# Kernel optimization log

Hardware: AMD Instinct MI355X
Metric: run time of the kernel (lower is better)

## Reference

```python
import jax, jax.numpy as jnp
import numpy as np

NEG = -9.0e15
D = 768


def _init_params(key, d):
    ks = jax.random.split(key, 12)
    s = 0.02
    p = {}
    p['Wa'] = jax.random.normal(ks[0], (d, 1), jnp.float32) * s
    p['ba'] = jnp.zeros((1,), jnp.float32)
    for i, name in enumerate(['qs', 'ks', 'qc', 'kc', 'qr', 'kr']):
        p['W' + name] = jax.random.normal(ks[1 + i], (d, d), jnp.float32) * s
        p['b' + name] = jnp.zeros((d,), jnp.float32)
    p['Wf1'] = jax.random.normal(ks[8], (3 * d, d), jnp.float32) * s
    p['bf1'] = jnp.zeros((d,), jnp.float32)
    p['Wf2'] = jax.random.normal(ks[9], (d, d), jnp.float32) * s
    p['bf2'] = jnp.zeros((d,), jnp.float32)
    p['gamma'] = jnp.ones((d,), jnp.float32)
    p['beta'] = jnp.zeros((d,), jnp.float32)
    return p


def setup_inputs() -> dict:
    key = jax.random.key(0)
    k1, k2, k3 = jax.random.split(key, 3)
    B, L = 8, 1024
    inp = {
        'x': jax.random.normal(k1, (B, L, D), jnp.float32),
        'x_ids': jax.random.randint(k2, (B, L), 0, 1000, jnp.int64 if jax.config.read('jax_enable_x64') else jnp.int32).astype(jnp.int32),
        'pad_idx': 0,
    }
    inp.update(_init_params(k3, D))
    return inp


def _forward(x, x_ids, pad_idx, Wa, ba, Wqs, bqs, Wks, bks, Wqc, bqc, Wkc, bkc,
             Wqr, bqr, Wkr, bkr, Wf1, bf1, Wf2, bf2, gamma, beta):
    B, L, d = x.shape
    valid = x_ids != pad_idx                             # [B,L]
    valid_len = valid.sum(axis=1)
    sep_pos = jnp.clip(valid_len // 2, 1, max(1, L - 2))  # [B]
    pos = jnp.arange(L)[None, :]                          # [1,L]
    false_mask = (pos < sep_pos[:, None]) & valid         # [B,L]
    option_mask = (pos > sep_pos[:, None]) & valid        # [B,L]

    # anomaly gate over false segment
    a_logits = (x @ Wa + ba)[..., 0]                      # [B,L]
    a_logits = jnp.where(false_mask, a_logits, NEG)
    gate = jax.nn.softmax(a_logits, axis=1) * false_mask.astype(x.dtype)
    gate = gate / jnp.clip(gate.sum(axis=1, keepdims=True), 1e-8)

    scale = 1.0 / jnp.sqrt(jnp.asarray(d, x.dtype))
    q_sup, k_sup = x @ Wqs + bqs, x @ Wks + bks
    q_con, k_con = x @ Wqc + bqc, x @ Wkc + bkc
    q_rep, k_rep = x @ Wqr + bqr, x @ Wkr + bkr

    sup_s = jnp.einsum('bld,bmd->blm', q_sup, k_sup) * scale
    con_s = jnp.einsum('bld,bmd->blm', q_con, k_con) * scale
    rep_s = jnp.einsum('bld,bmd->blm', q_rep, k_rep) * scale

    pair_mask = false_mask[:, :, None] & option_mask[:, None, :]  # [B,L,L]
    sup_attn = jax.nn.softmax(jnp.where(pair_mask, sup_s, NEG), axis=-1)
    rep_attn = jax.nn.softmax(jnp.where(pair_mask, rep_s + jnp.tanh(con_s), NEG), axis=-1)

    rep_vec = jnp.einsum('blm,bmd->bld', rep_attn, x)
    sup_vec = jnp.einsum('blm,bmd->bld', sup_attn, x)

    anomaly_false = jnp.einsum('bl,bld->bd', gate, x)
    w_rep = jnp.einsum('bl,bld->bd', gate, rep_vec)
    w_sup = jnp.einsum('bl,bld->bd', gate, sup_vec)

    fused = jnp.concatenate([anomaly_false, w_rep, w_sup], axis=-1)
    fused = jnp.maximum(fused @ Wf1 + bf1, 0.0) @ Wf2 + bf2  # dropout = eval identity

    mu = fused.mean(axis=-1, keepdims=True)
    var = ((fused - mu) ** 2).mean(axis=-1, keepdims=True)
    fused = (fused - mu) / jnp.sqrt(var + 1e-5) * gamma + beta
    return fused


def reference(x, x_ids, pad_idx, Wa, ba, Wqs, bqs, Wks, bks, Wqc, bqc, Wkc, bkc,
              Wqr, bqr, Wkr, bkr, Wf1, bf1, Wf2, bf2, gamma, beta):
    return _forward(x, x_ids, pad_idx, Wa, ba, Wqs, bqs, Wks, bks, Wqc, bqc,
                    Wkc, bkc, Wqr, bqr, Wkr, bkr, Wf1, bf1, Wf2, bf2, gamma, beta)
```

## Files before the change

### kernel.cpp

```cpp
#include <hip/hip_runtime.h>
#include <math.h>

#define L 1024
#define NB 8
#define D 768
#define NEGV (-9.0e15f)
#define SCALE 0.036084391824351615f

typedef unsigned short u16;
typedef __attribute__((ext_vector_type(8))) short short8;
typedef __attribute__((ext_vector_type(4))) float float4v;
#define MFMA_BF16 __builtin_amdgcn_mfma_f32_16x16x32_bf16

__device__ __forceinline__ float b2f(u16 u) {
    union { unsigned int i; float f; } v; v.i = ((unsigned int)u) << 16; return v.f;
}
__device__ __forceinline__ u16 f2b(float f) {
    union { float fv; unsigned int i; } v; v.fv = f;
    unsigned int x = v.i;
    x += 0x7fffu + ((x >> 16) & 1u);
    return (u16)(x >> 16);
}
__device__ __forceinline__ float unpk(unsigned int w, int h) {
    return b2f((u16)(h ? (w >> 16) : (w & 0xffffu)));
// ... 259 lines not shown
        short8 fa[2][4], fb[2][4];
        #pragma unroll
        for (int p = 0; p < 2; ++p) {
            #pragma unroll
            for (int i = 0; i < 4; ++i)
                fa[p][i] = *(const short8*)&Ab[p * 4096 + (wm + i * 16 + lrow) * 32 + sq];
            #pragma unroll
            for (int j = 0; j < 4; ++j)
                fb[p][j] = *(const short8*)&Bb[p * 4096 + (wn + j * 16 + lrow) * 32 + sq];
        }
        asm volatile("s_waitcnt lgkmcnt(0)" ::: "memory");
        __builtin_amdgcn_sched_barrier(0);
        __builtin_amdgcn_s_barrier();
        if (t < 10) {
            int k0 = (t + 2) << 6;
            u16* Ad = As + cur * 8192;
            u16* Bd = Bs + cur * 8192;
            stage128_async(A, lda, r0, k0, Ad, tid);
            stage128_async(A, lda, r0, k0 + 32, Ad + 4096, tid);
            stage128_async(B, ldb, c0, k0, Bd, tid);
            stage128_async(B, ldb, c0, k0 + 32, Bd + 4096, tid);
        }
        #pragma unroll
        for (int p = 0; p < 2; ++p)
            #pragma unroll
            for (int i = 0; i < 4; ++i)
                #pragma unroll
                for (int j = 0; j < 4; ++j)
                    acc[i][j] = MFMA_BF16(fa[p][i], fb[p][j], acc[i][j], 0, 0, 0);
    }
}

__global__ __launch_bounds__(256) void kB(const void* x, const int* __restrict__ ids,
        const int* __restrict__ padp, const float* __restrict__ alog,
        float* __restrict__ gate, int* __restrict__ sepArr,
        float* __restrict__ af, float* __restrict__ wrep, float* __restrict__ wsup,
        float* __restrict__ hacc, float* __restrict__ oacc,
        float* __restrict__ csup, float* __restrict__ crep,
        const u16* __restrict__ xb, const float* __restrict__ w1,
        const float* __restrict__ c0f, float* __restrict__ tbuf,
        const u16* __restrict__ Wb, u16* __restrict__ Mt) {
    __shared__ __align__(16) u16 SMEM[24576];
    int bid = blockIdx.x;
    int tid = threadIdx.x;
    if (bid >= 8 && bid < 224) {
        int i = bid - 8;
        int p = i / 72, j = i % 72;
        int r0 = (j / 6) * 64, c0m = (j % 6) * 128;
        u16* As = SMEM;
        u16* Bs = SMEM + 8192;
        float4v acc[2][4];
        gemm64_cnt(Wb + (size_t)(2 * p + 1) * D * D, D, r0,
                   Wb + (size_t)(2 * p) * D * D, D, c0m, As, Bs, acc);
        int lane = tid & 63, wave = tid >> 6;
        int wm = (wave >> 1) << 5, wn = (wave & 1) << 6;
        int quad = lane >> 4, lrow = lane & 15;
        u16* out = Mt + (size_t)p * D * D;
        #pragma unroll
        for (int ii = 0; ii < 2; ++ii)
            #pragma unroll
            for (int jj = 0; jj < 4; ++jj) {
                int brow = r0 + wm + ii * 16 + quad * 4;
                int col = c0m + wn + jj * 16 + lrow;
                #pragma unroll
                for (int r = 0; r < 4; ++r)
                    out[(size_t)(brow + r) * D + col] = f2b(acc[ii][jj][r]);
            }
        return;
    }
    if (bid >= 224) {
        int i = bid - 224;
        int b = i >> 2, q = i & 3;
        float* w1s = (float*)SMEM;
        for (int j = tid; j < D; j += 256) w1s[j] = w1[j];
        __syncthreads();
        float c0v = c0f[0];
        int sub = tid & 15;
        int rowi = tid >> 4;
        for (int pass = 0; pass < 8; ++pass) {
            int l = q * 128 + pass * 16 + rowi;
            const u16* xr = xb + ((size_t)b * L + l) * D;
            float a = 0.f;
            #pragma unroll
            for (int i2 = 0; i2 < 6; ++i2) {
                int k = i2 * 128 + sub * 8;
                short8 v = *(const short8*)&xr[k];
                #pragma unroll
                for (int e = 0; e < 8; ++e) a += b2f((u16)v[e]) * w1s[k + e];
            }
            #pragma unroll
            for (int d2 = 1; d2 < 16; d2 <<= 1) a += __shfl_xor(a, d2);
            if (sub == 0) tbuf[b * 512 + l] = a + c0v;
        }
        return;
    }
    float* red = (float*)SMEM;
    int*   ish = (int*)(red + 256);
    detect2(x, ids, ish);
    int is64 = ish[1];
    int b = bid;
    int pad = padp[0];
    int cnt = 0;
    for (int l = tid; l < L; l += 256) cnt += (ldid(ids, (size_t)b * L + l, is64) != pad) ? 1 : 0;
    red[tid] = (float)cnt; __syncthreads();
    for (int s = 128; s > 0; s >>= 1) { if (tid < s) red[tid] += red[tid + s]; __syncthreads(); }
    if (tid == 0) {
        int vl = (int)red[0];
        int sep = vl / 2; if (sep < 1) sep = 1; if (sep > L - 2) sep = L - 2;
        ish[2] = sep; sepArr[b] = sep;
    }
    __syncthreads();
    int sep = ish[2];
    float lv[4]; int lidx[4];
    float mx = -3.4e38f;
    for (int u = 0; u < 4; ++u) {
        int l = tid + u * 256; lidx[u] = l;
        bool fm = (l < sep) && (ldid(ids, (size_t)b * L + l, is64) != pad);
        float v = fm ? alog[b * L + l] : NEGV;
        lv[u] = v; mx = fmaxf(mx, v);
    }
    red[tid] = mx; __syncthreads();
    for (int s = 128; s > 0; s >>= 1) { if (tid < s) red[tid] = fmaxf(red[tid], red[tid + s]); __syncthreads(); }
    mx = red[0]; __syncthreads();
    float se = 0.f;
    for (int u = 0; u < 4; ++u) { lv[u] = expf(lv[u] - mx); se += lv[u]; }
    red[tid] = se; __syncthreads();
    for (int s = 128; s > 0; s >>= 1) { if (tid < s) red[tid] += red[tid + s]; __syncthreads(); }
    float den = fmaxf(red[0], 1e-30f); __syncthreads();
    float gs = 0.f; float gv[4];
    for (int u = 0; u < 4; ++u) {
        int l = lidx[u];
        bool fm = (l < sep) && (ldid(ids, (size_t)b * L + l, is64) != pad);
        float p = lv[u] / den;
        gv[u] = fm ? p : 0.f;
        gs += gv[u];
    }
    red[tid] = gs; __syncthreads();
    for (int s = 128; s > 0; s >>= 1) { if (tid < s) red[tid] += red[tid + s]; __syncthreads(); }
    gs = red[0];
    float inv = 1.f / fmaxf(gs, 1e-8f);
    for (int u = 0; u < 4; ++u) gate[b * L + lidx[u]] = gv[u] * inv;
    for (int l = tid; l < L; l += 256) { csup[b * L + l] = 0.f; crep[b * L + l] = 0.f; }
    for (int i = tid; i < D; i += 256) {
        af[b * D + i] = 0.f; wrep[b * D + i] = 0.f; wsup[b * D + i] = 0.f;
        hacc[b * D + i] = 0.f; oacc[b * D + i] = 0.f;
    }
}

__global__ __launch_bounds__(256) void kZ_mfma(const u16* __restrict__ xb,
        const u16* __restrict__ Mt, const float* __restrict__ z0,
        u16* __restrict__ Zbuf, const int* __restrict__ sepArr) {
    __shared__ __align__(16) u16 As[16384];
    __shared__ __align__(16) u16 Bs[16384];
    int z = blockIdx.z;
    int p = z >> 3, b = z & 7;
    int sep = sepArr[b];
    int r0 = blockIdx.y * 128;
    if (r0 >= sep) return;
    int c0 = blockIdx.x * 128;
    float4v acc[4][4];
    gemm128_cnt(xb + (size_t)b * L * D, D, r0,
                Mt + (size_t)p * D * D, D, c0, As, Bs, acc);
    int lane = threadIdx.x & 63, wave = threadIdx.x >> 6;
    int wm = (wave >> 1) << 6, wn = (wave & 1) << 6;
    int quad = lane >> 4, lrow = lane & 15;
    const float* z0p = z0 + p * D;
    u16* out = Zbuf + ((size_t)p * NB + b) * 512 * D;
    #pragma unroll
    for (int i = 0; i < 4; ++i)
        #pragma unroll
        for (int j = 0; j < 4; ++j) {
            int brow = r0 + wm + i * 16 + quad * 4;
            int col = c0 + wn + j * 16 + lrow;
            float zb = z0p[col];
            #pragma unroll
            for (int r = 0; r < 4; ++r)
                out[(size_t)(brow + r) * D + col] = f2b(acc[i][j][r] + zb);
        }
}

__device__ __forceinline__ void stageS(const u16* __restrict__ A0,
        const u16* __restrict__ A1, const u16* __restrict__ A2,
        const u16* __restrict__ X, int l0, int m0, int k0, u16* S, int tid) {
    #pragma unroll
    for (int r = 0; r < 3; ++r) {
        int slot = r * 256 + tid;
        int cs = slot < 704 ? slot : 703;
        const u16* g;
        if (cs < 192) {
            int m = cs >> 6, w2 = cs & 63, row = w2 >> 2, sub = w2 & 3;
            int subsw = sub ^ (row & 3);
            const u16* Am = (m == 0) ? A0 : (m == 1) ? A1 : A2;
            g = &Am[(size_t)(l0 + row) * D + k0 + subsw * 8];
        } else {
            int s2 = cs - 192, row = s2 >> 2, sub = s2 & 3;
            int subsw = sub ^ (row & 3);
            g = &X[(size_t)(m0 + row) * D + k0 + subsw * 8];
        }
        __builtin_amdgcn_global_load_lds((__attribute__((address_space(1))) void*)(u16*)g,
            (__attribute__((address_space(3))) void*)(S + ((r * 256 + (tid & 192)) * 8)), 16, 0, 0);
    }
}

__global__ __launch_bounds__(256) void kS2(const u16* __restrict__ Zbuf,
        const u16* __restrict__ xb, const float* __restrict__ tcbuf,
        const int* __restrict__ sepArr, const int* __restrict__ ids,
        const int* __restrict__ padp, const float* __restrict__ gate,
        float* __restrict__ csup, float* __restrict__ crep) {
    __shared__ __align__(16) u16 STG[18432];
    __shared__ float redmx[2][4][16];
    __shared__ float redsm[2][4][16];
    __shared__ int ish[1];
    int b = blockIdx.y;
    int sep = sepArr[b];
    int l0 = blockIdx.x * 16;
    if (l0 >= sep) return;
    int tid = threadIdx.x, lane = tid & 63, wave = tid >> 6;
    int lrow = lane & 15, quad = lane >> 4;
    if (tid < 64) {
        int v = ((const int*)ids)[tid * 2 + 1];
        unsigned long long bali = __ballot(v != 0);
        if (tid == 0) ish[0] = (bali == 0ULL) ? 1 : 0;
    }
    __syncthreads();
    int is64 = ish[0];
    int pad = padp[0];
    int msta = ((sep + 1) >> 7) << 7;
    int nchunk = (L - msta) >> 7;
    const u16* A0 = Zbuf + (size_t)b * 512 * D;
    const u16* A1 = Zbuf + ((size_t)NB + b) * 512 * D;
    const u16* A2 = Zbuf + ((size_t)2 * NB + b) * 512 * D;
    const u16* X  = xb + (size_t)b * L * D;
    float tcv[4], gr[4];
    #pragma unroll
    for (int r = 0; r < 4; ++r) {
        tcv[r] = tcbuf[b * 512 + l0 + quad * 4 + r];
        gr[r]  = gate[b * L + l0 + quad * 4 + r];
    }
    unsigned int pS[8][2][2], pC[8][2][2];
    int sq8 = ((quad ^ (lrow & 3)) << 3);
    #pragma unroll
    for (int c = 0; c < 8; ++c) {
      if (c < nchunk) {
        int m0c = msta + c * 128;
        float4v acc[3][2];
        #pragma unroll
        for (int m = 0; m < 3; ++m)
            #pragma unroll
            for (int j = 0; j < 2; ++j) acc[m][j] = (float4v){0.f, 0.f, 0.f, 0.f};
        stageS(A0, A1, A2, X, l0, m0c, 0,  STG, tid);
        stageS(A0, A1, A2, X, l0, m0c, 32, STG + 6144, tid);
        stageS(A0, A1, A2, X, l0, m0c, 64, STG + 12288, tid);
        #pragma unroll 1
        for (int t = 0; t < 24; ++t) {
            int cur = t - (t / 3) * 3;
            if (t < 22)       asm volatile("s_waitcnt vmcnt(6)" ::: "memory");
            else if (t == 22) asm volatile("s_waitcnt vmcnt(3)" ::: "memory");
            else              asm volatile("s_waitcnt vmcnt(0)" ::: "memory");
            __builtin_amdgcn_s_barrier();
            const u16* Sb = STG + cur * 6144;
            short8 fA0 = *(const short8*)&Sb[lrow * 32 + sq8];
            short8 fA1 = *(const short8*)&Sb[512 + lrow * 32 + sq8];
            short8 fA2 = *(const short8*)&Sb[1024 + lrow * 32 + sq8];
            int rB = wave * 32 + lrow;
            short8 fB0 = *(const short8*)&Sb[1536 + rB * 32 + sq8];
            short8 fB1 = *(const short8*)&Sb[1536 + (rB + 16) * 32 + sq8];
            asm volatile("s_waitcnt lgkmcnt(0)" ::: "memory");
            __builtin_amdgcn_sched_barrier(0);
            __builtin_amdgcn_s_barrier();
            if (t < 21) stageS(A0, A1, A2, X, l0, m0c, (t + 3) * 32, STG + cur * 6144, tid);
            acc[0][0] = MFMA_BF16(fA0, fB0, acc[0][0], 0, 0, 0);
            acc[0][1] = MFMA_BF16(fA0, fB1, acc[0][1], 0, 0, 0);
            acc[1][0] = MFMA_BF16(fA1, fB0, acc[1][0], 0, 0, 0);
            acc[1][1] = MFMA_BF16(fA1, fB1, acc[1][1], 0, 0, 0);
            acc[2][0] = MFMA_BF16(fA2, fB0, acc[2][0], 0, 0, 0);
            acc[2][1] = MFMA_BF16(fA2, fB1, acc[2][1], 0, 0, 0);
        }
        #pragma unroll
        for (int j = 0; j < 2; ++j) {
            int m = m0c + wave * 32 + j * 16 + lrow;
            bool ok = (m > sep) && (ldid(ids, (size_t)b * L + m, is64) != pad);
            float vs[4], vc[4];
            #pragma unroll
            for (int r = 0; r < 4; ++r) {
                vs[r] = ok ? acc[0][j][r] * SCALE : NEGV;
                vc[r] = ok ? (acc[2][j][r] * SCALE
                              + tanhf((acc[1][j][r] + tcv[r]) * SCALE)) : NEGV;
            }
            pS[c][j][0] = (unsigned)f2b(vs[0]) | ((unsigned)f2b(vs[1]) << 16);
            pS[c][j][1] = (unsigned)f2b(vs[2]) | ((unsigned)f2b(vs[3]) << 16);
            pC[c][j][0] = (unsigned)f2b(vc[0]) | ((unsigned)f2b(vc[1]) << 16);
            pC[c][j][1] = (unsigned)f2b(vc[2]) | ((unsigned)f2b(vc[3]) << 16);
        }
      }
    }
    float mxs[4], mxc[4];
    #pragma unroll
    for (int r = 0; r < 4; ++r) { mxs[r] = -3.4e38f; mxc[r] = -3.4e38f; }
    #pragma unroll
    for (int c = 0; c < 8; ++c) if (c < nchunk)
        #pragma unroll
        for (int j = 0; j < 2; ++j)
            #pragma unroll
            for (int r = 0; r < 4; ++r) {
                mxs[r] = fmaxf(mxs[r], unpk(pS[c][j][r >> 1], r & 1));
                mxc[r] = fmaxf(mxc[r], unpk(pC[c][j][r >> 1], r & 1));
            }
    #pragma unroll
    for (int d = 1; d < 16; d <<= 1)
        #pragma unroll
        for (int r = 0; r < 4; ++r) {
            mxs[r] = fmaxf(mxs[r], __shfl_xor(mxs[r], d));
            mxc[r] = fmaxf(mxc[r], __shfl_xor(mxc[r], d));
        }
    if (lrow == 0)
        #pragma unroll
        for (int r = 0; r < 4; ++r) {
            redmx[0][wave][quad * 4 + r] = mxs[r];
            redmx[1][wave][quad * 4 + r] = mxc[r];
        }
    __syncthreads();
    #pragma unroll
    for (int r = 0; r < 4; ++r) {
        int rr = quad * 4 + r;
        mxs[r] = fmaxf(fmaxf(redmx[0][0][rr], redmx[0][1][rr]),
                       fmaxf(redmx[0][2][rr], redmx[0][3][rr]));
        mxc[r] = fmaxf(fmaxf(redmx[1][0][rr], redmx[1][1][rr]),
                       fmaxf(redmx[1][2][rr], redmx[1][3][rr]));
    }
    float sms[4], smc[4];
    #pragma unroll
    for (int r = 0; r < 4; ++r) { sms[r] = 0.f; smc[r] = 0.f; }
    #pragma unroll
    for (int c = 0; c < 8; ++c) if (c < nchunk)
        #pragma unroll
        for (int j = 0; j < 2; ++j)
            #pragma unroll
            for (int r = 0; r < 4; ++r) {
                sms[r] += expf(unpk(pS[c][j][r >> 1], r & 1) - mxs[r]);
                smc[r] += expf(unpk(pC[c][j][r >> 1], r & 1) - mxc[r]);
            }
    #pragma unroll
    for (int d = 1; d < 16; d <<= 1)
        #pragma unroll
        for (int r = 0; r < 4; ++r) {
            sms[r] += __shfl_xor(sms[r], d);
            smc[r] += __shfl_xor(smc[r], d);
        }
    if (lrow == 0)
        #pragma unroll
        for (int r = 0; r < 4; ++r) {
            redsm[0][wave][quad * 4 + r] = sms[r];
            redsm[1][wave][quad * 4 + r] = smc[r];
        }
    __syncthreads();
    float wgs[4], wgc[4];
    #pragma unroll
    for (int r = 0; r < 4; ++r) {
        int rr = quad * 4 + r;
        float ds = redsm[0][0][rr] + redsm[0][1][rr] + redsm[0][2][rr] + redsm[0][3][rr];
        float dc = redsm[1][0][rr] + redsm[1][1][rr] + redsm[1][2][rr] + redsm[1][3][rr];
        wgs[r] = gr[r] / fmaxf(ds, 1e-30f);
        wgc[r] = gr[r] / fmaxf(dc, 1e-30f);
    }
    #pragma unroll
    for (int c = 0; c < 8; ++c) if (c < nchunk) {
        int m0c = msta + c * 128;
        #pragma unroll
        for (int j = 0; j < 2; ++j) {
            float as = 0.f, ar = 0.f;
            #pragma unroll
            for (int r = 0; r < 4; ++r) {
                as += wgs[r] * expf(unpk(pS[c][j][r >> 1], r & 1) - mxs[r]);
                ar += wgc[r] * expf(unpk(pC[c][j][r >> 1], r & 1) - mxc[r]);
            }
            as += __shfl_xor(as, 16); as += __shfl_xor(as, 32);
            ar += __shfl_xor(ar, 16); ar += __shfl_xor(ar, 32);
            if (quad == 0) {
                int m = m0c + wave * 32 + j * 16 + lrow;
                atomicAdd(&csup[b * L + m], as);
                atomicAdd(&crep[b * L + m], ar);
            }
        }
    }
}

__global__ __launch_bounds__(256) void k3(const u16* __restrict__ xb,
        const float* __restrict__ gate, const float* __restrict__ csup,
        const float* __restrict__ crep, float* __restrict__ af,
        float* __restrict__ wrep, float* __restrict__ wsup) {
    int b = blockIdx.y, c = blockIdx.x;
    int tid = threadIdx.x;
    float a0 = 0.f, a1 = 0.f, a2 = 0.f;
    float r0 = 0.f, r1 = 0.f, r2 = 0.f;
    float q0 = 0.f, q1 = 0.f, q2 = 0.f;
    for (int mm = 0; mm < 16; ++mm) {
        int m = c * 16 + mm;
        float wg = gate[b * L + m], wr = crep[b * L + m], wq = csup[b * L + m];
        if (wg == 0.f && wr == 0.f && wq == 0.f) continue;
        size_t base = ((size_t)b * L + m) * D;
        float x0 = b2f(xb[base + tid]);
        float x1 = b2f(xb[base + tid + 256]);
        float x2 = b2f(xb[base + tid + 512]);
        a0 += wg * x0; a1 += wg * x1; a2 += wg * x2;
        r0 += wr * x0; r1 += wr * x1; r2 += wr * x2;
        q0 += wq * x0; q1 += wq * x1; q2 += wq * x2;
    }
    atomicAdd(&af[b * D + tid], a0); atomicAdd(&af[b * D + tid + 256], a1); atomicAdd(&af[b * D + tid + 512], a2);
    atomicAdd(&wrep[b * D + tid], r0); atomicAdd(&wrep[b * D + tid + 256], r1); atomicAdd(&wrep[b * D + tid + 512], r2);
    atomicAdd(&wsup[b * D + tid], q0); atomicAdd(&wsup[b * D + tid + 256], q1); atomicAdd(&wsup[b * D + tid + 512], q2);
}

template<int F32> __device__ void kh1_body(const float* af, const float* wrep,
        const float* wsup, const void* Wf1, float* hacc, float* fs) {
    int tid = threadIdx.x;
    int c0 = blockIdx.x * 128, k0 = blockIdx.y * 144;
    for (int e = tid; e < 8 * 144; e += 256) {
        int b = e / 144, kk = e - b * 144;
        int k = k0 + kk;
        float v = (k < D) ? af[b * D + k] : (k < 2 * D) ? wrep[b * D + k - D]
                                                        : wsup[b * D + k - 2 * D];
        fs[b * 144 + kk] = v;
    }
    __syncthreads();
    int col = c0 + (tid & 127);
    int kg = tid >> 7;
    float acc[NB];
    #pragma unroll
    for (int b = 0; b < NB; ++b) acc[b] = 0.f;
    #pragma unroll 4
    for (int r = 0; r < 72; ++r) {
        int kk = kg * 72 + r;
        float w = ld1<F32>(Wf1, (size_t)(k0 + kk) * D + col);
        #pragma unroll
        for (int b = 0; b < NB; ++b) acc[b] += fs[b * 144 + kk] * w;
    }
    #pragma unroll
    for (int b = 0; b < NB; ++b) atomicAdd(&hacc[b * D + col], acc[b]);
}
__global__ __launch_bounds__(256) void kh1(const void* x, const int* ids,
        const float* af, const float* wrep,
        const float* wsup, const void* Wf1, float* hacc) {
    __shared__ float fs[8 * 144];
    __shared__ int fsh[2];
    detect2(x, ids, fsh);
    if (fsh[0]) kh1_body<1>(af, wrep, wsup, Wf1, hacc, fs);
    else        kh1_body<0>(af, wrep, wsup, Wf1, hacc, fs);
}

template<int F32> __device__ void kh2_body(const float* hacc, const void* bf1,
        const void* Wf2, float* oacc, float* hsl) {
    int tid = threadIdx.x;
    int c0 = blockIdx.x * 128, k0 = blockIdx.y * 96;
    for (int e = tid; e < 8 * 96; e += 256) {
        int b = e / 96, kk = e - b * 96;
        int k = k0 + kk;
        hsl[b * 96 + kk] = fmaxf(hacc[b * D + k] + ld1<F32>(bf1, k), 0.f);
    }
    __syncthreads();
    int col = c0 + (tid & 127);
    int kg = tid >> 7;
    float acc[NB];
    #pragma unroll
    for (int b = 0; b < NB; ++b) acc[b] = 0.f;
    #pragma unroll 4
    for (int r = 0; r < 48; ++r) {
        int kk = kg * 48 + r;
        float w = ld1<F32>(Wf2, (size_t)(k0 + kk) * D + col);
        #pragma unroll
        for (int b = 0; b < NB; ++b) acc[b] += hsl[b * 96 + kk] * w;
    }
    #pragma unroll
    for (int b = 0; b < NB; ++b) atomicAdd(&oacc[b * D + col], acc[b]);
}
__global__ __launch_bounds__(256) void kh2(const void* x, const int* ids,
        const float* hacc, const void* bf1,
        const void* Wf2, float* oacc) {
    __shared__ float hsl[8 * 96];
    __shared__ int fsh[2];
    detect2(x, ids, fsh);
    if (fsh[0]) kh2_body<1>(hacc, bf1, Wf2, oacc, hsl);
    else        kh2_body<0>(hacc, bf1, Wf2, oacc, hsl);
}

template<int F32> __device__ void kln_body(const float* oacc, const void* bf2,
        const void* gamma, const void* beta, void* out, float* red) {
    int b = blockIdx.x, tid = threadIdx.x;
    float o[3];
    #pragma unroll
    for (int u = 0; u < 3; ++u) {
        int i = tid + u * 256;
        o[u] = oacc[b * D + i] + ld1<F32>(bf2, i);
    }
    red[tid] = o[0] + o[1] + o[2]; __syncthreads();
    for (int s = 128; s > 0; s >>= 1) { if (tid < s) red[tid] += red[tid + s]; __syncthreads(); }
    float mu = red[0] / (float)D; __syncthreads();
    float vs = 0.f;
    #pragma unroll
    for (int u = 0; u < 3; ++u) vs += (o[u] - mu) * (o[u] - mu);
    red[tid] = vs; __syncthreads();
    for (int s = 128; s > 0; s >>= 1) { if (tid < s) red[tid] += red[tid + s]; __syncthreads(); }
    float var = red[0] / (float)D;
    float rstd = 1.0f / sqrtf(var + 1e-5f);
    #pragma unroll
    for (int u = 0; u < 3; ++u) {
        int i = tid + u * 256;
        float v = (o[u] - mu) * rstd * ld1<F32>(gamma, i) + ld1<F32>(beta, i);
        if (F32) ((float*)out)[b * D + i] = v;
        else     ((u16*)out)[b * D + i] = f2b(v);
    }
}
__global__ __launch_bounds__(256) void kln(const void* x, const int* ids,
        const float* oacc, const void* bf2,
        const void* gamma, const void* beta, void* out) {
    __shared__ float red[256];
    __shared__ int fsh[2];
    detect2(x, ids, fsh);
    if (fsh[0]) kln_body<1>(oacc, bf2, gamma, beta, out, red);
    else        kln_body<0>(oacc, bf2, gamma, beta, out, red);
}

extern "C" void kernel_launch(void* const* d_in, const int* in_sizes, int n_in,
                              void* d_out, int out_size, void* d_ws, size_t ws_size,
                              hipStream_t stream) {
    const void* x    = d_in[0];
    const int* ids   = (const int*)d_in[1];
    const int* padp  = (const int*)d_in[2];
    const void* Wa   = d_in[3];
    const void* ba   = d_in[4];
    PP pp;
    pp.W[0] = d_in[5];  pp.b[0] = d_in[6];
    pp.W[1] = d_in[7];  pp.b[1] = d_in[8];
    pp.W[2] = d_in[9];  pp.b[2] = d_in[10];
    pp.W[3] = d_in[11]; pp.b[3] = d_in[12];
    pp.W[4] = d_in[13]; pp.b[4] = d_in[14];
    pp.W[5] = d_in[15]; pp.b[5] = d_in[16];
    const void* Wf1 = d_in[17]; const void* bf1 = d_in[18];
    const void* Wf2 = d_in[19]; const void* bf2 = d_in[20];
    const void* gamma = d_in[21]; const void* beta = d_in[22];

    char* ws = (char*)d_ws;
    int*   sepArr = (int*)(ws + WS_SEP);
    float* c0   = (float*)(ws + WS_C0);
    float* z0   = (float*)(ws + WS_Z0);
    float* w1   = (float*)(ws + WS_W1);
    float* gate = (float*)(ws + WS_GATE);
    float* csup = (float*)(ws + WS_CSUP);
    float* crep = (float*)(ws + WS_CREP);
    float* af   = (float*)(ws + WS_AF);
    float* wrep = (float*)(ws + WS_WREP);
    float* wsup = (float*)(ws + WS_WSUP);
    float* hacc = (float*)(ws + WS_HACC);
    float* oacc = (float*)(ws + WS_OACC);
    float* alog = (float*)(ws + WS_ALOG);
    float* tbuf = (float*)(ws + WS_T);
    u16* xb   = (u16*)(ws + WS_XB);
    u16* Zbuf = (u16*)(ws + WS_Z);
    u16* Wb   = (u16*)(ws + WS_WB);
    u16* Mt   = (u16*)(ws + WS_M);

    kx<<<dim3(2044), dim3(256), 0, stream>>>(x, ids, pp, Wa, ba, xb, Wb, alog, z0, w1, c0);
    kB<<<dim3(256), dim3(256), 0, stream>>>(x, ids, padp, alog, gate, sepArr,
                                            af, wrep, wsup, hacc, oacc, csup, crep,
                                            xb, w1, c0, tbuf, Wb, Mt);
    kZ_mfma<<<dim3(6, 4, 24), dim3(256), 0, stream>>>(xb, Mt, z0, Zbuf, sepArr);
    kS2<<<dim3(32, NB), dim3(256), 0, stream>>>(Zbuf, xb, tbuf, sepArr, ids, padp,
                                                gate, csup, crep);
    k3<<<dim3(64, NB), dim3(256), 0, stream>>>(xb, gate, csup, crep, af, wrep, wsup);
    kh1<<<dim3(6, 16), dim3(256), 0, stream>>>(x, ids, af, wrep, wsup, Wf1, hacc);
    kh2<<<dim3(6, 8), dim3(256), 0, stream>>>(x, ids, hacc, bf1, Wf2, oacc);
    kln<<<dim3(NB), dim3(256), 0, stream>>>(x, ids, oacc, bf2, gamma, beta, d_out);
}
```

Baseline: 266.2 us.

## Split kS2 K-dimension across two wave groups with direct global fragment loads

kS2 now runs 512-thread blocks where two groups of four waves each compute half of the 768-long K reduction and merge partial MFMA accumulators through shared memory. The LDS-staged triple-buffered pipeline is replaced by direct global loads of bf16 fragments into registers. Both kZ_mfma and kS2 use flattened 1D grids with the batch index in the low bits, which spreads batches across CUs. The intent is more waves in flight to hide latency and better balance across batches, at the cost of uncoalesced fragment loads, no LDS reuse, and extra barriers for the reduction.

Result: slower. 282.5 us (+6.1%).

```diff
diff --git a/kernel.cpp b/kernel.cpp
--- a/kernel.cpp
+++ b/kernel.cpp
@@ -435,12 +435,15 @@
         u16* __restrict__ Zbuf, const int* __restrict__ sepArr) {
     __shared__ __align__(16) u16 As[16384];
     __shared__ __align__(16) u16 Bs[16384];
-    int z = blockIdx.z;
-    int p = z >> 3, b = z & 7;
+    int bid = blockIdx.x;
+    int b = bid & 7;
+    int r = bid >> 3;
+    int p = r / 24;
+    int rr = r % 24;
+    int r0 = (rr / 6) * 128;
+    int c0 = (rr % 6) * 128;
     int sep = sepArr[b];
-    int r0 = blockIdx.y * 128;
     if (r0 >= sep) return;
-    int c0 = blockIdx.x * 128;
     float4v acc[4][4];
     gemm128_cnt(xb + (size_t)b * L * D, D, r0,
                 Mt + (size_t)p * D * D, D, c0, As, Bs, acc);
@@ -457,55 +460,34 @@
             int col = c0 + wn + j * 16 + lrow;
             float zb = z0p[col];
             #pragma unroll
-            for (int r = 0; r < 4; ++r)
-                out[(size_t)(brow + r) * D + col] = f2b(acc[i][j][r] + zb);
-        }
-}
-
-__device__ __forceinline__ void stageS(const u16* __restrict__ A0,
-        const u16* __restrict__ A1, const u16* __restrict__ A2,
-        const u16* __restrict__ X, int l0, int m0, int k0, u16* S, int tid) {
-    #pragma unroll
-    for (int r = 0; r < 3; ++r) {
-        int slot = r * 256 + tid;
-        int cs = slot < 704 ? slot : 703;
-        const u16* g;
-        if (cs < 192) {
-            int m = cs >> 6, w2 = cs & 63, row = w2 >> 2, sub = w2 & 3;
-            int subsw = sub ^ (row & 3);
-            const u16* Am = (m == 0) ? A0 : (m == 1) ? A1 : A2;
-            g = &Am[(size_t)(l0 + row) * D + k0 + subsw * 8];
-        } else {
-            int s2 = cs - 192, row = s2 >> 2, sub = s2 & 3;
-            int subsw = sub ^ (row & 3);
-            g = &X[(size_t)(m0 + row) * D + k0 + subsw * 8];
-        }
-        __builtin_amdgcn_global_load_lds((__attribute__((address_space(1))) void*)(u16*)g,
-            (__attribute__((address_space(3))) void*)(S + ((r * 256 + (tid & 192)) * 8)), 16, 0, 0);
-    }
-}
-
-__global__ __launch_bounds__(256) void kS2(const u16* __restrict__ Zbuf,
+            for (int r2 = 0; r2 < 4; ++r2)
+                out[(size_t)(brow + r2) * D + col] = f2b(acc[i][j][r2] + zb);
+        }
+}
+
+__global__ __launch_bounds__(512) void kS2(const u16* __restrict__ Zbuf,
         const u16* __restrict__ xb, const float* __restrict__ tcbuf,
         const int* __restrict__ sepArr, const int* __restrict__ ids,
         const int* __restrict__ padp, const float* __restrict__ gate,
         float* __restrict__ csup, float* __restrict__ crep) {
-    __shared__ __align__(16) u16 STG[18432];
+    __shared__ float REDB[4][64][24];
     __shared__ float redmx[2][4][16];
     __shared__ float redsm[2][4][16];
     __shared__ int ish[1];
-    int b = blockIdx.y;
+    int bid = blockIdx.x;
+    int b = bid & 7;
+    int l0 = (bid >> 3) * 16;
     int sep = sepArr[b];
-    int l0 = blockIdx.x * 16;
-    if (l0 >= sep) return;
     int tid = threadIdx.x, lane = tid & 63, wave = tid >> 6;
     int lrow = lane & 15, quad = lane >> 4;
+    int cg = wave & 3, kq = wave >> 2;
     if (tid < 64) {
         int v = ((const int*)ids)[tid * 2 + 1];
         unsigned long long bali = __ballot(v != 0);
         if (tid == 0) ish[0] = (bali == 0ULL) ? 1 : 0;
     }
     __syncthreads();
+    if (l0 >= sep) return;
     int is64 = ish[0];
     int pad = padp[0];
     int msta = ((sep + 1) >> 7) << 7;
@@ -514,6 +496,10 @@
     const u16* A1 = Zbuf + ((size_t)NB + b) * 512 * D;
     const u16* A2 = Zbuf + ((size_t)2 * NB + b) * 512 * D;
     const u16* X  = xb + (size_t)b * L * D;
+    size_t aoff = (size_t)(l0 + lrow) * D + kq * 384 + quad * 8;
+    const u16* pA0 = A0 + aoff;
+    const u16* pA1 = A1 + aoff;
+    const u16* pA2 = A2 + aoff;
     float tcv[4], gr[4];
     #pragma unroll
     for (int r = 0; r < 4; ++r) {
@@ -521,37 +507,25 @@
         gr[r]  = gate[b * L + l0 + quad * 4 + r];
     }
     unsigned int pS[8][2][2], pC[8][2][2];
-    int sq8 = ((quad ^ (lrow & 3)) << 3);
     #pragma unroll
     for (int c = 0; c < 8; ++c) {
       if (c < nchunk) {
         int m0c = msta + c * 128;
+        const u16* pB0 = X + (size_t)(m0c + cg * 32 + lrow) * D + kq * 384 + quad * 8;
+        const u16* pB1 = pB0 + (size_t)16 * D;
         float4v acc[3][2];
         #pragma unroll
         for (int m = 0; m < 3; ++m)
             #pragma unroll
             for (int j = 0; j < 2; ++j) acc[m][j] = (float4v){0.f, 0.f, 0.f, 0.f};
-        stageS(A0, A1, A2, X, l0, m0c, 0,  STG, tid);
-        stageS(A0, A1, A2, X, l0, m0c, 32, STG + 6144, tid);
-        stageS(A0, A1, A2, X, l0, m0c, 64, STG + 12288, tid);
-        #pragma unroll 1
-        for (int t = 0; t < 24; ++t) {
-            int cur = t - (t / 3) * 3;
-            if (t < 22)       asm volatile("s_waitcnt vmcnt(6)" ::: "memory");
-            else if (t == 22) asm volatile("s_waitcnt vmcnt(3)" ::: "memory");
-            else              asm volatile("s_waitcnt vmcnt(0)" ::: "memory");
-            __builtin_amdgcn_s_barrier();
-            const u16* Sb = STG + cur * 6144;
-            short8 fA0 = *(const short8*)&Sb[lrow * 32 + sq8];
-            short8 fA1 = *(const short8*)&Sb[512 + lrow * 32 + sq8];
-            short8 fA2 = *(const short8*)&Sb[1024 + lrow * 32 + sq8];
-            int rB = wave * 32 + lrow;
-            short8 fB0 = *(const short8*)&Sb[1536 + rB * 32 + sq8];
-            short8 fB1 = *(const short8*)&Sb[1536 + (rB + 16) * 32 + sq8];
-            asm volatile("s_waitcnt lgkmcnt(0)" ::: "memory");
-            __builtin_amdgcn_sched_barrier(0);
-            __builtin_amdgcn_s_barrier();
-            if (t < 21) stageS(A0, A1, A2, X, l0, m0c, (t + 3) * 32, STG + cur * 6144, tid);
+        #pragma unroll
+        for (int s = 0; s < 12; ++s) {
+            int ko = s * 32;
+            short8 fA0 = *(const short8*)(pA0 + ko);
+            short8 fA1 = *(const short8*)(pA1 + ko);
+            short8 fA2 = *(const short8*)(pA2 + ko);
+            short8 fB0 = *(const short8*)(pB0 + ko);
+            short8 fB1 = *(const short8*)(pB1 + ko);
             acc[0][0] = MFMA_BF16(fA0, fB0, acc[0][0], 0, 0, 0);
             acc[0][1] = MFMA_BF16(fA0, fB1, acc[0][1], 0, 0, 0);
             acc[1][0] = MFMA_BF16(fA1, fB0, acc[1][0], 0, 0, 0);
@@ -559,110 +533,131 @@
             acc[2][0] = MFMA_BF16(fA2, fB0, acc[2][0], 0, 0, 0);
             acc[2][1] = MFMA_BF16(fA2, fB1, acc[2][1], 0, 0, 0);
         }
-        #pragma unroll
-        for (int j = 0; j < 2; ++j) {
-            int m = m0c + wave * 32 + j * 16 + lrow;
-            bool ok = (m > sep) && (ldid(ids, (size_t)b * L + m, is64) != pad);
-            float vs[4], vc[4];
+        __syncthreads();
+        if (kq == 1) {
+            #pragma unroll
+            for (int m = 0; m < 3; ++m)
+                #pragma unroll
+                for (int j = 0; j < 2; ++j)
+                    *(float4v*)&REDB[cg][lane][(m * 2 + j) * 4] = acc[m][j];
+        }
+        __syncthreads();
+        if (kq == 0) {
+            #pragma unroll
+            for (int m = 0; m < 3; ++m)
+                #pragma unroll
+                for (int j = 0; j < 2; ++j)
+                    acc[m][j] += *(const float4v*)&REDB[cg][lane][(m * 2 + j) * 4];
+            #pragma unroll
+            for (int j = 0; j < 2; ++j) {
+                int m = m0c + cg * 32 + j * 16 + lrow;
+                bool ok = (m > sep) && (ldid(ids, (size_t)b * L + m, is64) != pad);
+                float vs[4], vc[4];
+                #pragma unroll
+                for (int r = 0; r < 4; ++r) {
+                    vs[r] = ok ? acc[0][j][r] * SCALE : NEGV;
+                    vc[r] = ok ? (acc[2][j][r] * SCALE
+                                  + tanhf((acc[1][j][r] + tcv[r]) * SCALE)) : NEGV;
+                }
+                pS[c][j][0] = (unsigned)f2b(vs[0]) | ((unsigned)f2b(vs[1]) << 16);
+                pS[c][j][1] = (unsigned)f2b(vs[2]) | ((unsigned)f2b(vs[3]) << 16);
+                pC[c][j][0] = (unsigned)f2b(vc[0]) | ((unsigned)f2b(vc[1]) << 16);
+                pC[c][j][1] = (unsigned)f2b(vc[2]) | ((unsigned)f2b(vc[3]) << 16);
+            }
+        }
+      }
+    }
+    float mxs[4], mxc[4];
+    if (wave < 4) {
+        #pragma unroll
+        for (int r = 0; r < 4; ++r) { mxs[r] = -3.4e38f; mxc[r] = -3.4e38f; }
+        #pragma unroll
+        for (int c = 0; c < 8; ++c) if (c < nchunk)
+            #pragma unroll
+            for (int j = 0; j < 2; ++j)
+                #pragma unroll
+                for (int r = 0; r < 4; ++r) {
+                    mxs[r] = fmaxf(mxs[r], unpk(pS[c][j][r >> 1], r & 1));
+                    mxc[r] = fmaxf(mxc[r], unpk(pC[c][j][r >> 1], r & 1));
+                }
+        #pragma unroll
+        for (int d = 1; d < 16; d <<= 1)
             #pragma unroll
             for (int r = 0; r < 4; ++r) {
-                vs[r] = ok ? acc[0][j][r] * SCALE : NEGV;
-                vc[r] = ok ? (acc[2][j][r] * SCALE
-                              + tanhf((acc[1][j][r] + tcv[r]) * SCALE)) : NEGV;
+                mxs[r] = fmaxf(mxs[r], __shfl_xor(mxs[r], d));
+                mxc[r] = fmaxf(mxc[r], __shfl_xor(mxc[r], d));
             }
-            pS[c][j][0] = (unsigned)f2b(vs[0]) | ((unsigned)f2b(vs[1]) << 16);
-            pS[c][j][1] = (unsigned)f2b(vs[2]) | ((unsigned)f2b(vs[3]) << 16);
-            pC[c][j][0] = (unsigned)f2b(vc[0]) | ((unsigned)f2b(vc[1]) << 16);
-            pC[c][j][1] = (unsigned)f2b(vc[2]) | ((unsigned)f2b(vc[3]) << 16);
-        }
-      }
-    }
-    float mxs[4], mxc[4];
-    #pragma unroll
-    for (int r = 0; r < 4; ++r) { mxs[r] = -3.4e38f; mxc[r] = -3.4e38f; }
-    #pragma unroll
-    for (int c = 0; c < 8; ++c) if (c < nchunk)
-        #pragma unroll
-        for (int j = 0; j < 2; ++j)
+        if (lrow == 0)
             #pragma unroll
             for (int r = 0; r < 4; ++r) {
-                mxs[r] = fmaxf(mxs[r], unpk(pS[c][j][r >> 1], r & 1));
-                mxc[r] = fmaxf(mxc[r], unpk(pC[c][j][r >> 1], r & 1));
+                redmx[0][cg][quad * 4 + r] = mxs[r];
+                redmx[1][cg][quad * 4 + r] = mxc[r];
             }
-    #pragma unroll
-    for (int d = 1; d < 16; d <<= 1)
+    }
+    __syncthreads();
+    float sms[4], smc[4];
+    if (wave < 4) {
         #pragma unroll
         for (int r = 0; r < 4; ++r) {
-            mxs[r] = fmaxf(mxs[r], __shfl_xor(mxs[r], d));
-            mxc[r] = fmaxf(mxc[r], __shfl_xor(mxc[r], d));
-        }
-    if (lrow == 0)
+            int rr = quad * 4 + r;
+            mxs[r] = fmaxf(fmaxf(redmx[0][0][rr], redmx[0][1][rr]),
+                           fmaxf(redmx[0][2][rr], redmx[0][3][rr]));
+            mxc[r] = fmaxf(fmaxf(redmx[1][0][rr], redmx[1][1][rr]),
+                           fmaxf(redmx[1][2][rr], redmx[1][3][rr]));
+            sms[r] = 0.f; smc[r] = 0.f;
+        }
+        #pragma unroll
+        for (int c = 0; c < 8; ++c) if (c < nchunk)
+            #pragma unroll
+            for (int j = 0; j < 2; ++j)
+                #pragma unroll
+                for (int r = 0; r < 4; ++r) {
+                    sms[r] += expf(unpk(pS[c][j][r >> 1], r & 1) - mxs[r]);
+                    smc[r] += expf(unpk(pC[c][j][r >> 1], r & 1) - mxc[r]);
+                }
+        #pragma unroll
+        for (int d = 1; d < 16; d <<= 1)
+            #pragma unroll
+            for (int r = 0; r < 4; ++r) {
+                sms[r] += __shfl_xor(sms[r], d);
+                smc[r] += __shfl_xor(smc[r], d);
+            }
+        if (lrow == 0)
+            #pragma unroll
+            for (int r = 0; r < 4; ++r) {
+                redsm[0][cg][quad * 4 + r] = sms[r];
+                redsm[1][cg][quad * 4 + r] = smc[r];
+            }
+    }
+    __syncthreads();
+    if (wave < 4) {
+        float wgs[4], wgc[4];
         #pragma unroll
         for (int r = 0; r < 4; ++r) {
-            redmx[0][wave][quad * 4 + r] = mxs[r];
-            redmx[1][wave][quad * 4 + r] = mxc[r];
-        }
-    __syncthreads();
-    #pragma unroll
-    for (int r = 0; r < 4; ++r) {
-        int rr = quad * 4 + r;
-        mxs[r] = fmaxf(fmaxf(redmx[0][0][rr], redmx[0][1][rr]),
-                       fmaxf(redmx[0][2][rr], redmx[0][3][rr]));
-        mxc[r] = fmaxf(fmaxf(redmx[1][0][rr], redmx[1][1][rr]),
-                       fmaxf(redmx[1][2][rr], redmx[1][3][rr]));
-    }
-    float sms[4], smc[4];
-    #pragma unroll
-    for (int r = 0; r < 4; ++r) { sms[r] = 0.f; smc[r] = 0.f; }
-    #pragma unroll
-    for (int c = 0; c < 8; ++c) if (c < nchunk)
-        #pragma unroll
-        for (int j = 0; j < 2; ++j)
-            #pragma unroll
-            for (int r = 0; r < 4; ++r) {
-                sms[r] += expf(unpk(pS[c][j][r >> 1], r & 1) - mxs[r]);
-                smc[r] += expf(unpk(pC[c][j][r >> 1], r & 1) - mxc[r]);
-            }
-    #pragma unroll
-    for (int d = 1; d < 16; d <<= 1)
-        #pragma unroll
-        for (int r = 0; r < 4; ++r) {
-            sms[r] += __shfl_xor(sms[r], d);
-            smc[r] += __shfl_xor(smc[r], d);
-        }
-    if (lrow == 0)
-        #pragma unroll
-        for (int r = 0; r < 4; ++r) {
-            redsm[0][wave][quad * 4 + r] = sms[r];
-            redsm[1][wave][quad * 4 + r] = smc[r];
-        }
-    __syncthreads();
-    float wgs[4], wgc[4];
-    #pragma unroll
-    for (int r = 0; r < 4; ++r) {
-        int rr = quad * 4 + r;
-        float ds = redsm[0][0][rr] + redsm[0][1][rr] + redsm[0][2][rr] + redsm[0][3][rr];
-        float dc = redsm[1][0][rr] + redsm[1][1][rr] + redsm[1][2][rr] + redsm[1][3][rr];
-        wgs[r] = gr[r] / fmaxf(ds, 1e-30f);
-        wgc[r] = gr[r] / fmaxf(dc, 1e-30f);
-    }
-    #pragma unroll
-    for (int c = 0; c < 8; ++c) if (c < nchunk) {
-        int m0c = msta + c * 128;
-        #pragma unroll
-        for (int j = 0; j < 2; ++j) {
-            float as = 0.f, ar = 0.f;
-            #pragma unroll
-            for (int r = 0; r < 4; ++r) {
-                as += wgs[r] * expf(unpk(pS[c][j][r >> 1], r & 1) - mxs[r]);
-                ar += wgc[r] * expf(unpk(pC[c][j][r >> 1], r & 1) - mxc[r]);
-            }
-            as += __shfl_xor(as, 16); as += __shfl_xor(as, 32);
-            ar += __shfl_xor(ar, 16); ar += __shfl_xor(ar, 32);
-            if (quad == 0) {
-                int m = m0c + wave * 32 + j * 16 + lrow;
-                atomicAdd(&csup[b * L + m], as);
-                atomicAdd(&crep[b * L + m], ar);
+            int rr = quad * 4 + r;
+            float ds = redsm[0][0][rr] + redsm[0][1][rr] + redsm[0][2][rr] + redsm[0][3][rr];
+            float dc = redsm[1][0][rr] + redsm[1][1][rr] + redsm[1][2][rr] + redsm[1][3][rr];
+            wgs[r] = gr[r] / fmaxf(ds, 1e-30f);
+            wgc[r] = gr[r] / fmaxf(dc, 1e-30f);
+        }
+        #pragma unroll
+        for (int c = 0; c < 8; ++c) if (c < nchunk) {
+            int m0c = msta + c * 128;
+            #pragma unroll
+            for (int j = 0; j < 2; ++j) {
+                float as = 0.f, ar = 0.f;
+                #pragma unroll
+                for (int r = 0; r < 4; ++r) {
+                    as += wgs[r] * expf(unpk(pS[c][j][r >> 1], r & 1) - mxs[r]);
+                    ar += wgc[r] * expf(unpk(pC[c][j][r >> 1], r & 1) - mxc[r]);
+                }
+                as += __shfl_xor(as, 16); as += __shfl_xor(as, 32);
+                ar += __shfl_xor(ar, 16); ar += __shfl_xor(ar, 32);
+                if (quad == 0) {
+                    int m = m0c + cg * 32 + j * 16 + lrow;
+                    atomicAdd(&csup[b * L + m], as);
+                    atomicAdd(&crep[b * L + m], ar);
+                }
             }
         }
     }
@@ -846,9 +841,9 @@
     kB<<<dim3(256), dim3(256), 0, stream>>>(x, ids, padp, alog, gate, sepArr,
                                             af, wrep, wsup, hacc, oacc, csup, crep,
                                             xb, w1, c0, tbuf, Wb, Mt);
-    kZ_mfma<<<dim3(6, 4, 24), dim3(256), 0, stream>>>(xb, Mt, z0, Zbuf, sepArr);
-    kS2<<<dim3(32, NB), dim3(256), 0, stream>>>(Zbuf, xb, tbuf, sepArr, ids, padp,
-                                                gate, csup, crep);
+    kZ_mfma<<<dim3(576), dim3(256), 0, stream>>>(xb, Mt, z0, Zbuf, sepArr);
+    kS2<<<dim3(256), dim3(512), 0, stream>>>(Zbuf, xb, tbuf, sepArr, ids, padp,
+                                             gate, csup, crep);
     k3<<<dim3(64, NB), dim3(256), 0, stream>>>(xb, gate, csup, crep, af, wrep, wsup);
     kh1<<<dim3(6, 16), dim3(256), 0, stream>>>(x, ids, af, wrep, wsup, Wf1, hacc);
     kh2<<<dim3(6, 8), dim3(256), 0, stream>>>(x, ids, hacc, bf1, Wf2, oacc);
```

## Drop LDS staging in kS2, load MFMA fragments directly from global with 8 waves

Applied to the files above, without the earlier changes.

Removes the triple-buffered global_load_lds staging pipeline and its barriers in the score kernel. Each lane now loads its bf16 fragments straight from global memory. Blocks grow to 512 threads (8 waves), each wave covers 16 key rows across four chunks at once, and the grid is flattened with the batch index interleaved. The aim is to cut barrier and LDS overhead and raise parallelism, at the cost of losing shared reuse of the A tile and X rows across waves, which relies on the L1/L2 caches instead.

Result: faster. 258.6 us (-2.8%).

```diff
diff --git a/kernel.cpp b/kernel.cpp
--- a/kernel.cpp
+++ b/kernel.cpp
@@ -462,42 +462,18 @@
         }
 }
 
-__device__ __forceinline__ void stageS(const u16* __restrict__ A0,
-        const u16* __restrict__ A1, const u16* __restrict__ A2,
-        const u16* __restrict__ X, int l0, int m0, int k0, u16* S, int tid) {
-    #pragma unroll
-    for (int r = 0; r < 3; ++r) {
-        int slot = r * 256 + tid;
-        int cs = slot < 704 ? slot : 703;
-        const u16* g;
-        if (cs < 192) {
-            int m = cs >> 6, w2 = cs & 63, row = w2 >> 2, sub = w2 & 3;
-            int subsw = sub ^ (row & 3);
-            const u16* Am = (m == 0) ? A0 : (m == 1) ? A1 : A2;
-            g = &Am[(size_t)(l0 + row) * D + k0 + subsw * 8];
-        } else {
-            int s2 = cs - 192, row = s2 >> 2, sub = s2 & 3;
-            int subsw = sub ^ (row & 3);
-            g = &X[(size_t)(m0 + row) * D + k0 + subsw * 8];
-        }
-        __builtin_amdgcn_global_load_lds((__attribute__((address_space(1))) void*)(u16*)g,
-            (__attribute__((address_space(3))) void*)(S + ((r * 256 + (tid & 192)) * 8)), 16, 0, 0);
-    }
-}
-
-__global__ __launch_bounds__(256) void kS2(const u16* __restrict__ Zbuf,
+__global__ __launch_bounds__(512) void kS2(const u16* __restrict__ Zbuf,
         const u16* __restrict__ xb, const float* __restrict__ tcbuf,
         const int* __restrict__ sepArr, const int* __restrict__ ids,
         const int* __restrict__ padp, const float* __restrict__ gate,
         float* __restrict__ csup, float* __restrict__ crep) {
-    __shared__ __align__(16) u16 STG[18432];
-    __shared__ float redmx[2][4][16];
-    __shared__ float redsm[2][4][16];
+    __shared__ float redmx[2][8][16];
+    __shared__ float redsm[2][8][16];
     __shared__ int ish[1];
-    int b = blockIdx.y;
+    int bid = blockIdx.x;
+    int b = bid & 7;
+    int l0 = (bid >> 3) * 16;
     int sep = sepArr[b];
-    int l0 = blockIdx.x * 16;
-    if (l0 >= sep) return;
     int tid = threadIdx.x, lane = tid & 63, wave = tid >> 6;
     int lrow = lane & 15, quad = lane >> 4;
     if (tid < 64) {
@@ -506,13 +482,15 @@
         if (tid == 0) ish[0] = (bali == 0ULL) ? 1 : 0;
     }
     __syncthreads();
+    if (l0 >= sep) return;
     int is64 = ish[0];
     int pad = padp[0];
     int msta = ((sep + 1) >> 7) << 7;
     int nchunk = (L - msta) >> 7;
-    const u16* A0 = Zbuf + (size_t)b * 512 * D;
-    const u16* A1 = Zbuf + ((size_t)NB + b) * 512 * D;
-    const u16* A2 = Zbuf + ((size_t)2 * NB + b) * 512 * D;
+    size_t aoff = (size_t)(l0 + lrow) * D + quad * 8;
+    const u16* pA0 = Zbuf + (size_t)b * 512 * D + aoff;
+    const u16* pA1 = Zbuf + ((size_t)NB + b) * 512 * D + aoff;
+    const u16* pA2 = Zbuf + ((size_t)2 * NB + b) * 512 * D + aoff;
     const u16* X  = xb + (size_t)b * L * D;
     float tcv[4], gr[4];
     #pragma unroll
@@ -520,60 +498,63 @@
         tcv[r] = tcbuf[b * 512 + l0 + quad * 4 + r];
         gr[r]  = gate[b * L + l0 + quad * 4 + r];
     }
-    unsigned int pS[8][2][2], pC[8][2][2];
-    int sq8 = ((quad ^ (lrow & 3)) << 3);
-    #pragma unroll
-    for (int c = 0; c < 8; ++c) {
-      if (c < nchunk) {
-        int m0c = msta + c * 128;
-        float4v acc[3][2];
+    unsigned int pS[8][2], pC[8][2];
+    #pragma unroll
+    for (int g = 0; g < 2; ++g) {
+      if (g * 4 < nchunk) {
+        const u16* pB[4];
+        #pragma unroll
+        for (int cc = 0; cc < 4; ++cc) {
+            int m0c = msta + (g * 4 + cc) * 128;
+            if (m0c > L - 128) m0c = L - 128;
+            pB[cc] = X + (size_t)(m0c + wave * 16 + lrow) * D + quad * 8;
+        }
+        float4v acc[3][4];
         #pragma unroll
         for (int m = 0; m < 3; ++m)
             #pragma unroll
-            for (int j = 0; j < 2; ++j) acc[m][j] = (float4v){0.f, 0.f, 0.f, 0.f};
-        stageS(A0, A1, A2, X, l0, m0c, 0,  STG, tid);
-        stageS(A0, A1, A2, X, l0, m0c, 32, STG + 6144, tid);
-        stageS(A0, A1, A2, X, l0, m0c, 64, STG + 12288, tid);
-        #pragma unroll 1
-        for (int t = 0; t < 24; ++t) {
-            int cur = t - (t / 3) * 3;
-            if (t < 22)       asm volatile("s_waitcnt vmcnt(6)" ::: "memory");
-            else if (t == 22) asm volatile("s_waitcnt vmcnt(3)" ::: "memory");
-            else              asm volatile("s_waitcnt vmcnt(0)" ::: "memory");
-            __builtin_amdgcn_s_barrier();
-            const u16* Sb = STG + cur * 6144;
-            short8 fA0 = *(const short8*)&Sb[lrow * 32 + sq8];
-            short8 fA1 = *(const short8*)&Sb[512 + lrow * 32 + sq8];
-            short8 fA2 = *(const short8*)&Sb[1024 + lrow * 32 + sq8];
-            int rB = wave * 32 + lrow;
-            short8 fB0 = *(const short8*)&Sb[1536 + rB * 32 + sq8];
-            short8 fB1 = *(const short8*)&Sb[1536 + (rB + 16) * 32 + sq8];
-            asm volatile("s_waitcnt lgkmcnt(0)" ::: "memory");
-            __builtin_amdgcn_sched_barrier(0);
-            __builtin_amdgcn_s_barrier();
-            if (t < 21) stageS(A0, A1, A2, X, l0, m0c, (t + 3) * 32, STG + cur * 6144, tid);
+            for (int cc = 0; cc < 4; ++cc) acc[m][cc] = (float4v){0.f, 0.f, 0.f, 0.f};
+        #pragma unroll
+        for (int s = 0; s < 24; ++s) {
+            int ko = s * 32;
+            short8 fA0 = *(const short8*)(pA0 + ko);
+            short8 fA1 = *(const short8*)(pA1 + ko);
+            short8 fA2 = *(const short8*)(pA2 + ko);
+            short8 fB0 = *(const short8*)(pB[0] + ko);
+            short8 fB1 = *(const short8*)(pB[1] + ko);
+            short8 fB2 = *(const short8*)(pB[2] + ko);
+            short8 fB3 = *(const short8*)(pB[3] + ko);
             acc[0][0] = MFMA_BF16(fA0, fB0, acc[0][0], 0, 0, 0);
+            acc[1][0] = MFMA_BF16(fA1, fB0, acc[1][0], 0, 0, 0);
+            acc[2][0] = MFMA_BF16(fA2, fB0, acc[2][0], 0, 0, 0);
             acc[0][1] = MFMA_BF16(fA0, fB1, acc[0][1], 0, 0, 0);
-            acc[1][0] = MFMA_BF16(fA1, fB0, acc[1][0], 0, 0, 0);
             acc[1][1] = MFMA_BF16(fA1, fB1, acc[1][1], 0, 0, 0);
-            acc[2][0] = MFMA_BF16(fA2, fB0, acc[2][0], 0, 0, 0);
             acc[2][1] = MFMA_BF16(fA2, fB1, acc[2][1], 0, 0, 0);
-        }
-        #pragma unroll
-        for (int j = 0; j < 2; ++j) {
-            int m = m0c + wave * 32 + j * 16 + lrow;
-            bool ok = (m > sep) && (ldid(ids, (size_t)b * L + m, is64) != pad);
-            float vs[4], vc[4];
-            #pragma unroll
-            for (int r = 0; r < 4; ++r) {
-                vs[r] = ok ? acc[0][j][r] * SCALE : NEGV;
-                vc[r] = ok ? (acc[2][j][r] * SCALE
-                              + tanhf((acc[1][j][r] + tcv[r]) * SCALE)) : NEGV;
+            acc[0][2] = MFMA_BF16(fA0, fB2, acc[0][2], 0, 0, 0);
+            acc[1][2] = MFMA_BF16(fA1, fB2, acc[1][2], 0, 0, 0);
+            acc[2][2] = MFMA_BF16(fA2, fB2, acc[2][2], 0, 0, 0);
+            acc[0][3] = MFMA_BF16(fA0, fB3, acc[0][3], 0, 0, 0);
+            acc[1][3] = MFMA_BF16(fA1, fB3, acc[1][3], 0, 0, 0);
+            acc[2][3] = MFMA_BF16(fA2, fB3, acc[2][3], 0, 0, 0);
+        }
+        #pragma unroll
+        for (int cc = 0; cc < 4; ++cc) {
+            int c = g * 4 + cc;
+            if (c < nchunk) {
+                int m = msta + c * 128 + wave * 16 + lrow;
+                bool ok = (m > sep) && (ldid(ids, (size_t)b * L + m, is64) != pad);
+                float vs[4], vc[4];
+                #pragma unroll
+                for (int r = 0; r < 4; ++r) {
+                    vs[r] = ok ? acc[0][cc][r] * SCALE : NEGV;
+                    vc[r] = ok ? (acc[2][cc][r] * SCALE
+                                  + tanhf((acc[1][cc][r] + tcv[r]) * SCALE)) : NEGV;
+                }
+                pS[c][0] = (unsigned)f2b(vs[0]) | ((unsigned)f2b(vs[1]) << 16);
+                pS[c][1] = (unsigned)f2b(vs[2]) | ((unsigned)f2b(vs[3]) << 16);
+                pC[c][0] = (unsigned)f2b(vc[0]) | ((unsigned)f2b(vc[1]) << 16);
+                pC[c][1] = (unsigned)f2b(vc[2]) | ((unsigned)f2b(vc[3]) << 16);
             }
-            pS[c][j][0] = (unsigned)f2b(vs[0]) | ((unsigned)f2b(vs[1]) << 16);
-            pS[c][j][1] = (unsigned)f2b(vs[2]) | ((unsigned)f2b(vs[3]) << 16);
-            pC[c][j][0] = (unsigned)f2b(vc[0]) | ((unsigned)f2b(vc[1]) << 16);
-            pC[c][j][1] = (unsigned)f2b(vc[2]) | ((unsigned)f2b(vc[3]) << 16);
         }
       }
     }
@@ -583,12 +564,10 @@
     #pragma unroll
     for (int c = 0; c < 8; ++c) if (c < nchunk)
         #pragma unroll
-        for (int j = 0; j < 2; ++j)
-            #pragma unroll
-            for (int r = 0; r < 4; ++r) {
-                mxs[r] = fmaxf(mxs[r], unpk(pS[c][j][r >> 1], r & 1));
-                mxc[r] = fmaxf(mxc[r], unpk(pC[c][j][r >> 1], r & 1));
-            }
+        for (int r = 0; r < 4; ++r) {
+            mxs[r] = fmaxf(mxs[r], unpk(pS[c][r >> 1], r & 1));
+            mxc[r] = fmaxf(mxc[r], unpk(pC[c][r >> 1], r & 1));
+        }
     #pragma unroll
     for (int d = 1; d < 16; d <<= 1)
         #pragma unroll
@@ -606,10 +585,13 @@
     #pragma unroll
     for (int r = 0; r < 4; ++r) {
         int rr = quad * 4 + r;
-        mxs[r] = fmaxf(fmaxf(redmx[0][0][rr], redmx[0][1][rr]),
-                       fmaxf(redmx[0][2][rr], redmx[0][3][rr]));
-        mxc[r] = fmaxf(fmaxf(redmx[1][0][rr], redmx[1][1][rr]),
-                       fmaxf(redmx[1][2][rr], redmx[1][3][rr]));
+        float m0 = redmx[0][0][rr], m1 = redmx[1][0][rr];
+        #pragma unroll
+        for (int w = 1; w < 8; ++w) {
+            m0 = fmaxf(m0, redmx[0][w][rr]);
+            m1 = fmaxf(m1, redmx[1][w][rr]);
+        }
+        mxs[r] = m0; mxc[r] = m1;
     }
     float sms[4], smc[4];
     #pragma unroll
@@ -617,12 +599,10 @@
     #pragma unroll
     for (int c = 0; c < 8; ++c) if (c < nchunk)
         #pragma unroll
-        for (int j = 0; j < 2; ++j)
-            #pragma unroll
-            for (int r = 0; r < 4; ++r) {
-                sms[r] += expf(unpk(pS[c][j][r >> 1], r & 1) - mxs[r]);
-                smc[r] += expf(unpk(pC[c][j][r >> 1], r & 1) - mxc[r]);
-            }
+        for (int r = 0; r < 4; ++r) {
+            sms[r] += expf(unpk(pS[c][r >> 1], r & 1) - mxs[r]);
+            smc[r] += expf(unpk(pC[c][r >> 1], r & 1) - mxc[r]);
+        }
     #pragma unroll
     for (int d = 1; d < 16; d <<= 1)
         #pragma unroll
@@ -641,29 +621,29 @@
     #pragma unroll
     for (int r = 0; r < 4; ++r) {
         int rr = quad * 4 + r;
-        float ds = redsm[0][0][rr] + redsm[0][1][rr] + redsm[0][2][rr] + redsm[0][3][rr];
-        float dc = redsm[1][0][rr] + redsm[1][1][rr] + redsm[1][2][rr] + redsm[1][3][rr];
-        wgs[r] = gr[r] / fmaxf(ds, 1e-30f);
-        wgc[r] = gr[r] / fmaxf(dc, 1e-30f);
+        float d0 = redsm[0][0][rr], d1 = redsm[1][0][rr];
+        #pragma unroll
+        for (int w = 1; w < 8; ++w) {
+            d0 += redsm[0][w][rr];
+            d1 += redsm[1][w][rr];
+        }
+        wgs[r] = gr[r] / fmaxf(d0, 1e-30f);
+        wgc[r] = gr[r] / fmaxf(d1, 1e-30f);
     }
     #pragma unroll
     for (int c = 0; c < 8; ++c) if (c < nchunk) {
-        int m0c = msta + c * 128;
-        #pragma unroll
-        for (int j = 0; j < 2; ++j) {
-            float as = 0.f, ar = 0.f;
-            #pragma unroll
-            for (int r = 0; r < 4; ++r) {
-                as += wgs[r] * expf(unpk(pS[c][j][r >> 1], r & 1) - mxs[r]);
-                ar += wgc[r] * expf(unpk(pC[c][j][r >> 1], r & 1) - mxc[r]);
-            }
-            as += __shfl_xor(as, 16); as += __shfl_xor(as, 32);
-            ar += __shfl_xor(ar, 16); ar += __shfl_xor(ar, 32);
-            if (quad == 0) {
-                int m = m0c + wave * 32 + j * 16 + lrow;
-                atomicAdd(&csup[b * L + m], as);
-                atomicAdd(&crep[b * L + m], ar);
-            }
+        float as = 0.f, ar = 0.f;
+        #pragma unroll
+        for (int r = 0; r < 4; ++r) {
+            as += wgs[r] * expf(unpk(pS[c][r >> 1], r & 1) - mxs[r]);
+            ar += wgc[r] * expf(unpk(pC[c][r >> 1], r & 1) - mxc[r]);
+        }
+        as += __shfl_xor(as, 16); as += __shfl_xor(as, 32);
+        ar += __shfl_xor(ar, 16); ar += __shfl_xor(ar, 32);
+        if (quad == 0) {
+            int m = msta + c * 128 + wave * 16 + lrow;
+            atomicAdd(&csup[b * L + m], as);
+            atomicAdd(&crep[b * L + m], ar);
         }
     }
 }
@@ -847,8 +827,8 @@
                                             af, wrep, wsup, hacc, oacc, csup, crep,
                                             xb, w1, c0, tbuf, Wb, Mt);
     kZ_mfma<<<dim3(6, 4, 24), dim3(256), 0, stream>>>(xb, Mt, z0, Zbuf, sepArr);
-    kS2<<<dim3(32, NB), dim3(256), 0, stream>>>(Zbuf, xb, tbuf, sepArr, ids, padp,
-                                                gate, csup, crep);
+    kS2<<<dim3(256), dim3(512), 0, stream>>>(Zbuf, xb, tbuf, sepArr, ids, padp,
+                                             gate, csup, crep);
     k3<<<dim3(64, NB), dim3(256), 0, stream>>>(xb, gate, csup, crep, af, wrep, wsup);
     kh1<<<dim3(6, 16), dim3(256), 0, stream>>>(x, ids, af, wrep, wsup, Wf1, hacc);
     kh2<<<dim3(6, 8), dim3(256), 0, stream>>>(x, ids, hacc, bf1, Wf2, oacc);
```
